# Kernel tuning notes

Hardware: AMD Instinct MI355X
Metric: run time of the kernel (lower is better)

## Reference

```python
import jax, jax.numpy as jnp
import numpy as np

ALPHA = 0.2        # LeakyReLU slope for attention scores (init arg alpha)
MLP_ALPHA = 0.01   # torch nn.LeakyReLU default slope in aftermlp
EPS = 1e-5         # nn.LayerNorm default eps


def leaky(x, a):
    return jnp.where(x >= 0, x, a * x)


def setup_inputs() -> dict:
    key = jax.random.key(0)
    ks = jax.random.split(key, 12)
    B, N, FIN, FOUT, K = 4, 4096, 256, 256, 64
    s = 0.05
    return {
        "h": jax.random.normal(ks[0], (B, N, FIN), jnp.float32),
        "adj": jax.random.uniform(ks[1], (B, N, N), jnp.float32),
        "W": jax.random.normal(ks[2], (FIN, FOUT), jnp.float32) * s,
        "a": jax.random.normal(ks[3], (FOUT, 1), jnp.float32) * s,
        "ln_g": jnp.ones((FOUT,), jnp.float32),
        "ln_b": jnp.zeros((FOUT,), jnp.float32),
        "W1": jax.random.normal(ks[4], (FOUT, FOUT), jnp.float32) * s,
        "b1": jnp.zeros((FOUT,), jnp.float32),
        "W2": jax.random.normal(ks[5], (FOUT, FOUT), jnp.float32) * s,
        "b2": jnp.zeros((FOUT,), jnp.float32),
        "W3": jax.random.normal(ks[6], (FOUT, FOUT), jnp.float32) * s,
        "b3": jnp.zeros((FOUT,), jnp.float32),
        "k": K,
    }


def reference(h, adj, W, a, ln_g, ln_b, W1, b1, W2, b2, W3, b3, k):
    # Wh: [B, N, F]
    Wh = h @ W
    B, N, Fd = Wh.shape
    C = N // k
    Whc = Wh.reshape(B, C, k, Fd)                       # [B, C, k, F]
    # a_input[b,c,i,j] = Wh[b,c,i]  =>  e[b,c,i,j] = leaky(Wh[b,c,i] . a)
    e = leaky(jnp.squeeze(Whc @ a, -1), ALPHA)          # [B, C, k]
    # block-diagonal chunks of adj: [B, C, k, k]
    idx = jnp.arange(C)
    blocks = adj.reshape(B, C, k, C, k)[:, idx, :, idx, :]  # [C, B, k, k]
    blocks = jnp.transpose(blocks, (1, 0, 2, 3))            # [B, C, k, k]
    scores = jax.nn.softmax(blocks * e[..., :, None], axis=-1)  # [B, C, k, k]
    out = jnp.einsum('bcij,bcjf->bcif', scores, Whc)    # [B, C, k, F]
    # aftermlp: Linear -> LeakyReLU(0.01) -> Linear -> LeakyReLU(0.01) -> Linear
    y = leaky(out @ W1 + b1, MLP_ALPHA)
    y = leaky(y @ W2 + b2, MLP_ALPHA)
    y = y @ W3 + b3
    # residual + LayerNorm over last dim
    z = y + out
    mu = jnp.mean(z, axis=-1, keepdims=True)
    var = jnp.var(z, axis=-1, keepdims=True)
    z = (z - mu) / jnp.sqrt(var + EPS) * ln_g + ln_b
    return z.reshape(B, N, Fd)
```

## Files before the change

kernel.cpp:

```cpp
#include <hip/hip_runtime.h>

typedef __bf16 bf16;
typedef __bf16 bf16x4 __attribute__((ext_vector_type(4)));
typedef __bf16 bf16x8 __attribute__((ext_vector_type(8)));
typedef float  f32x4  __attribute__((ext_vector_type(4)));

#define ALPHA 0.2f
#define MLP_ALPHA 0.01f
#define LN_EPS 1e-5f

constexpr int Bb = 4;
constexpr int Nn = 4096;
constexpr int Ff = 256;
constexpr int Kk = 64;
constexpr int Cc = 64;

__device__ __forceinline__ f32x4 MFMA(bf16x8 a, bf16x8 b, f32x4 c) {
  return __builtin_amdgcn_mfma_f32_16x16x32_bf16(a, b, c, 0, 0, 0);
}
__device__ __forceinline__ bf16x4 pack4(f32x4 v) {
  bf16x4 r; r[0]=(bf16)v[0]; r[1]=(bf16)v[1]; r[2]=(bf16)v[2]; r[3]=(bf16)v[3]; return r;
}
__device__ __forceinline__ int swz512(int i, int inrow) { return i*512 + (inrow ^ ((i & 15) << 4)); }
__device__ __forceinline__ int swz128(int f, int inrow) { return f*128 + (inrow ^ ((f & 7) << 4)); }

__global__ __launch_bounds__(256) void prep_weights(
    const float* __restrict__ W0, const float* __restrict__ W1,
    const float* __restrict__ W2, const float* __restrict__ W3,
    const float* __restrict__ a_vec,
    bf16* __restrict__ outw, float* __restrict__ wa)
{
  if (blockIdx.x == 128) {
    int k = threadIdx.x;
    const float* row = W0 + k * Ff;
    float s = 0.f;
    for (int j = 0; j < Ff; j += 4) {
      f32x4 wv = *(const f32x4*)(row + j);
      f32x4 av = *(const f32x4*)(a_vec + j);
      s += wv[0]*av[0] + wv[1]*av[1] + wv[2]*av[2] + wv[3]*av[3];
    }
    wa[k] = s;
    return;
  }
  int t = blockIdx.x * 256 + threadIdx.x;
  int l = t & 63, nt = (t >> 6) & 15, kt = (t >> 10) & 7, mat = t >> 13;
  const float* src = (mat==0) ? W0 : (mat==1) ? W1 : (mat==2) ? W2 : W3;
  int n  = nt*16 + (l & 15);
  int k0 = kt*32 + (l >> 4)*8;
  bf16x8 v;
  #pragma unroll
  for (int jj = 0; jj < 8; ++jj) v[jj] = (bf16)src[(k0 + jj)*Ff + n];
  *(bf16x8*)(outw + (size_t)t * 8) = v;
}

__device__ __forceinline__ void mlp_gemm(const bf16* __restrict__ wfrag, int mat,
                                         const bf16* inBuf, f32x4 acc[4][2],
                                         int w, int l)
{
  const int g = l >> 4, li = l & 15;
  #pragma unroll
  for (int kt = 0; kt < 8; ++kt) {
    bf16x8 af[2], bfr[4];
    #pragma unroll
    for (int r = 0; r < 2; ++r)
      af[r] = *(const bf16x8*)(wfrag + ((((size_t)mat*8 + kt)*16 + (w*2 + r))*64 + l)*8);
    #pragma unroll
    for (int nt = 0; nt < 4; ++nt) {
      int i = nt*16 + li;
      bfr[nt] = *(const bf16x8*)((const char*)inBuf + swz512(i, (kt*32 + g*8)*2));
    }
    #pragma unroll
    for (int nt = 0; nt < 4; ++nt)
      #pragma unroll
      for (int r = 0; r < 2; ++r)
        acc[nt][r] = MFMA(af[r], bfr[nt], acc[nt][r]);
  }
}

__device__ __forceinline__ void stage_store(f32x4 acc[4][2], const float* __restrict__ bias,
                                            bf16* outBuf, int w, int l)
{
  const int g = l >> 4, li = l & 15;
  float bv[2][4];
  #pragma unroll
  for (int r = 0; r < 2; ++r)
    #pragma unroll
    for (int e = 0; e < 4; ++e) bv[r][e] = bias[(w*2 + r)*16 + g*4 + e];
  #pragma unroll
  for (int nt = 0; nt < 4; ++nt) {
    int i = nt*16 + li;
    #pragma unroll
    for (int r = 0; r < 2; ++r) {
      f32x4 v;
      #pragma unroll
      for (int e = 0; e < 4; ++e) {
        float x = acc[nt][r][e] + bv[r][e];
        v[e] = (x >= 0.f) ? x : MLP_ALPHA * x;
      }
      int f0 = (w*2 + r)*16 + g*4;
      *(bf16x4*)((char*)outBuf + swz512(i, f0*2)) = pack4(v);
    }
  }
}

__global__ __launch_bounds__(512, 2) void gat_mfma(
    const float* __restrict__ h,   const float* __restrict__ adj,
    const float* __restrict__ gln, const float* __restrict__ bln,
    const float* __restrict__ b1,  const float* __restrict__ b2,
    const float* __restrict__ b3,
    const bf16* __restrict__ wfrag, const float* __restrict__ wa,
    float* __restrict__ out)
{
  __shared__ bf16 hbs[Kk * Ff];
  __shared__ bf16 bufA[Ff * Kk];
  __shared__ bf16 bufB[Kk * Ff];
  __shared__ bf16 sS[Kk * Kk];
  __shared__ float evec[Kk];
  __shared__ float lnS[Kk * 8], lnQ[Kk * 8];

  const int t = threadIdx.x, l = t & 63, w = t >> 6, g = l >> 4, li = l & 15;
  const int bc = blockIdx.x, b = bc >> 6, c = bc & 63;
  const size_t rbase = (size_t)b * Nn + c * Kk;

  float adjv[8];
  #pragma unroll
  for (int rr = 0; rr < 8; ++rr)
    adjv[rr] = adj[(rbase + w*8 + rr) * Nn + (size_t)c*Kk + l];

  {
    const int i  = t >> 3;
    const int k0 = (t & 7) * 32;
    const float* hp = h + (rbase + i) * Ff + k0;
    float p = 0.f;
    #pragma unroll
    for (int u = 0; u < 4; ++u) {
      f32x4 h0 = *(const f32x4*)(hp + u*8);
      f32x4 h1 = *(const f32x4*)(hp + u*8 + 4);
      f32x4 w0 = *(const f32x4*)(wa + k0 + u*8);
      f32x4 w1 = *(const f32x4*)(wa + k0 + u*8 + 4);
      p += h0[0]*w0[0] + h0[1]*w0[1] + h0[2]*w0[2] + h0[3]*w0[3]
         + h1[0]*w1[0] + h1[1]*w1[1] + h1[2]*w1[2] + h1[3]*w1[3];
      bf16x8 v;
      #pragma unroll
      for (int d = 0; d < 4; ++d) { v[d] = (bf16)h0[d]; v[4+d] = (bf16)h1[d]; }
      *(bf16x8*)((char*)hbs + swz512(i, (k0 + u*8)*2)) = v;
    }
    p += __shfl_xor(p, 1); p += __shfl_xor(p, 2); p += __shfl_xor(p, 4);
    if ((l & 7) == 0) evec[i] = (p >= 0.f) ? p : ALPHA * p;
  }
  __syncthreads();

  #pragma unroll
  for (int rr = 0; rr < 8; ++rr) {
    int i = w*8 + rr;
    float x = adjv[rr] * evec[i];
    float m = x;
    #pragma unroll
    for (int off = 32; off; off >>= 1) m = fmaxf(m, __shfl_xor(m, off));
    float pe = __expf(x - m);
    float s = pe;
    #pragma unroll
    for (int off = 32; off; off >>= 1) s += __shfl_xor(s, off);
    *(bf16*)((char*)sS + swz128(i, l*2)) = (bf16)(pe / s);
  }

  f32x4 acc1[2][4];
  #pragma unroll
  for (int q = 0; q < 2; ++q)
    #pragma unroll
    for (int rt = 0; rt < 4; ++rt) acc1[q][rt] = (f32x4){0.f,0.f,0.f,0.f};
  #pragma unroll
  for (int kt = 0; kt < 8; ++kt) {
    bf16x8 af[4];
    #pragma unroll
    for (int rt = 0; rt < 4; ++rt) {
      int i = rt*16 + li;
      af[rt] = *(const bf16x8*)((const char*)hbs + swz512(i, (kt*32 + g*8)*2));
    }
    #pragma unroll
    for (int q = 0; q < 2; ++q) {
      bf16x8 bfr = *(const bf16x8*)(wfrag + (((size_t)kt*16 + (w*2 + q))*64 + l)*8);
      #pragma unroll
      for (int rt = 0; rt < 4; ++rt) acc1[q][rt] = MFMA(af[rt], bfr, acc1[q][rt]);
    }
  }
  #pragma unroll
  for (int q = 0; q < 2; ++q) {
    int f = (w*2 + q)*16 + li;
    #pragma unroll
    for (int rt = 0; rt < 4; ++rt) {
      int j0 = rt*16 + g*4;
      *(bf16x4*)((char*)bufA + swz128(f, j0*2)) = pack4(acc1[q][rt]);
    }
  }
  __syncthreads();

  f32x4 xr[4][2];
  #pragma unroll
  for (int nt = 0; nt < 4; ++nt)
    #pragma unroll
    for (int r = 0; r < 2; ++r) xr[nt][r] = (f32x4){0.f,0.f,0.f,0.f};
  #pragma unroll
  for (int kt = 0; kt < 2; ++kt) {
    int koff = (kt*32 + g*8)*2;
    bf16x8 af[2], bfr[4];
    #pragma unroll
    for (int r = 0; r < 2; ++r) {
      int f = (w*2 + r)*16 + li;
      af[r] = *(const bf16x8*)((const char*)bufA + swz128(f, koff));
    }
    #pragma unroll
    for (int nt = 0; nt < 4; ++nt) {
      int i = nt*16 + li;
      bfr[nt] = *(const bf16x8*)((const char*)sS + swz128(i, koff));
    }
    #pragma unroll
    for (int nt = 0; nt < 4; ++nt)
      #pragma unroll
      for (int r = 0; r < 2; ++r) xr[nt][r] = MFMA(af[r], bfr[nt], xr[nt][r]);
  }
  #pragma unroll
  for (int nt = 0; nt < 4; ++nt) {
    int i = nt*16 + li;
    #pragma unroll
    for (int r = 0; r < 2; ++r) {
      int f0 = (w*2 + r)*16 + g*4;
      *(bf16x4*)((char*)bufB + swz512(i, f0*2)) = pack4(xr[nt][r]);
    }
  }
  __syncthreads();

  f32x4 acc3[4][2];
  #pragma unroll
  for (int nt = 0; nt < 4; ++nt)
    #pragma unroll
    for (int r = 0; r < 2; ++r) acc3[nt][r] = (f32x4){0.f,0.f,0.f,0.f};
  mlp_gemm(wfrag, 1, bufB, acc3, w, l);
  stage_store(acc3, b1, bufA, w, l);
  __syncthreads();

  #pragma unroll
  for (int nt = 0; nt < 4; ++nt)
    #pragma unroll
    for (int r = 0; r < 2; ++r) acc3[nt][r] = (f32x4){0.f,0.f,0.f,0.f};
  mlp_gemm(wfrag, 2, bufA, acc3, w, l);
  stage_store(acc3, b2, bufB, w, l);
  __syncthreads();

  #pragma unroll
  for (int nt = 0; nt < 4; ++nt)
    #pragma unroll
    for (int r = 0; r < 2; ++r) acc3[nt][r] = (f32x4){0.f,0.f,0.f,0.f};
  mlp_gemm(wfrag, 3, bufB, acc3, w, l);

  {
    float bv[2][4], gv[2][4], btv[2][4];
    #pragma unroll
    for (int r = 0; r < 2; ++r)
      #pragma unroll
      for (int e = 0; e < 4; ++e) {
        int f = (w*2 + r)*16 + g*4 + e;
        bv[r][e] = b3[f]; gv[r][e] = gln[f]; btv[r][e] = bln[f];
      }
    #pragma unroll
    for (int nt = 0; nt < 4; ++nt) {
      float s = 0.f, qq = 0.f;
      #pragma unroll
      for (int r = 0; r < 2; ++r)
        #pragma unroll
        for (int e = 0; e < 4; ++e) {
          float z = acc3[nt][r][e] + bv[r][e] + xr[nt][r][e];
          acc3[nt][r][e] = z;
          s += z; qq += z*z;
        }
      s  += __shfl_xor(s, 16);  s  += __shfl_xor(s, 32);
      qq += __shfl_xor(qq, 16); qq += __shfl_xor(qq, 32);
      if (g == 0) {
        int i = nt*16 + li;
        lnS[i*8 + w] = s;
        lnQ[i*8 + w] = qq;
      }
    }
    __syncthreads();
    #pragma unroll
    for (int nt = 0; nt < 4; ++nt) {
      int i = nt*16 + li;
      f32x4 s0 = *(const f32x4*)&lnS[i*8];
      f32x4 s1 = *(const f32x4*)&lnS[i*8 + 4];
      f32x4 q0 = *(const f32x4*)&lnQ[i*8];
      f32x4 q1 = *(const f32x4*)&lnQ[i*8 + 4];
      float s  = s0[0]+s0[1]+s0[2]+s0[3]+s1[0]+s1[1]+s1[2]+s1[3];
      float qq = q0[0]+q0[1]+q0[2]+q0[3]+q1[0]+q1[1]+q1[2]+q1[3];
      float mu  = s * (1.f/256.f);
      float var = qq * (1.f/256.f) - mu*mu;
      float rs  = rsqrtf(var + LN_EPS);
      #pragma unroll
      for (int r = 0; r < 2; ++r) {
        float4 o;
        o.x = (acc3[nt][r][0] - mu)*rs*gv[r][0] + btv[r][0];
        o.y = (acc3[nt][r][1] - mu)*rs*gv[r][1] + btv[r][1];
        o.z = (acc3[nt][r][2] - mu)*rs*gv[r][2] + btv[r][2];
        o.w = (acc3[nt][r][3] - mu)*rs*gv[r][3] + btv[r][3];
        *(float4*)&out[(rbase + i)*Ff + (w*2 + r)*16 + g*4] = o;
      }
    }
  }
}

extern "C" void kernel_launch(void* const* d_in, const int* in_sizes, int n_in,
                              void* d_out, int out_size, void* d_ws, size_t ws_size,
                              hipStream_t stream) {
  (void)in_sizes; (void)n_in; (void)out_size; (void)ws_size;
  bf16*  wfrag = (bf16*)d_ws;
  float* wa    = (float*)((char*)d_ws + 512*1024);
  prep_weights<<<dim3(129), dim3(256), 0, stream>>>(
      (const float*)d_in[2], (const float*)d_in[6],
      (const float*)d_in[8], (const float*)d_in[10],
      (const float*)d_in[3], wfrag, wa);
  gat_mfma<<<dim3(Bb * Cc), dim3(512), 0, stream>>>(
      (const float*)d_in[0],  (const float*)d_in[1],
      (const float*)d_in[4],  (const float*)d_in[5],
      (const float*)d_in[7],  (const float*)d_in[9],  (const float*)d_in[11],
      wfrag, wa, (float*)d_out);
}
```

Measured before the change: 36.82 us.

## Drop redundant barriers via shuffles and prefetch MLP weight fragments across syncs

The per-row attention scalar is now broadcast with a wavefront shuffle instead of going through shared memory, which removes one block-wide barrier. The barrier between writing bufA and the aggregation GEMM is also dropped, since each wave reads back only the rows it wrote. The first half of each MLP layer's weight fragments is loaded from global memory before the preceding barrier, so that load latency overlaps the sync wait. The cost is extra registers for the prefetched fragments, which could reduce occupancy at two blocks per CU.

```diff
diff --git a/kernel.cpp b/kernel.cpp
--- a/kernel.cpp
+++ b/kernel.cpp
@@ -53,53 +53,40 @@
   *(bf16x8*)(outw + (size_t)t * 8) = v;
 }
 
-__device__ __forceinline__ void mlp_gemm(const bf16* __restrict__ wfrag, int mat,
-                                         const bf16* inBuf, f32x4 acc[4][2],
-                                         int w, int l)
+__device__ __forceinline__ void prefetch_af(const bf16* __restrict__ wfrag, int mat,
+                                            bf16x8 pf[4][2], int w, int l) {
+  #pragma unroll
+  for (int kt = 0; kt < 4; ++kt)
+    #pragma unroll
+    for (int r = 0; r < 2; ++r)
+      pf[kt][r] = *(const bf16x8*)(wfrag + ((((size_t)mat*8 + kt)*16 + (w*2 + r))*64 + l)*8);
+}
+
+__device__ __forceinline__ void mlp_stage(const bf16* __restrict__ wfrag, int mat,
+                                          const bf16* inB, f32x4 acc[4][2],
+                                          bf16x8 pf[4][2], int w, int l)
 {
   const int g = l >> 4, li = l & 15;
   #pragma unroll
   for (int kt = 0; kt < 8; ++kt) {
-    bf16x8 af[2], bfr[4];
-    #pragma unroll
-    for (int r = 0; r < 2; ++r)
-      af[r] = *(const bf16x8*)(wfrag + ((((size_t)mat*8 + kt)*16 + (w*2 + r))*64 + l)*8);
+    bf16x8 af[2];
+    if (kt < 4) { af[0] = pf[kt][0]; af[1] = pf[kt][1]; }
+    else {
+      #pragma unroll
+      for (int r = 0; r < 2; ++r)
+        af[r] = *(const bf16x8*)(wfrag + ((((size_t)mat*8 + kt)*16 + (w*2 + r))*64 + l)*8);
+    }
+    bf16x8 bfr[4];
     #pragma unroll
     for (int nt = 0; nt < 4; ++nt) {
       int i = nt*16 + li;
-      bfr[nt] = *(const bf16x8*)((const char*)inBuf + swz512(i, (kt*32 + g*8)*2));
+      bfr[nt] = *(const bf16x8*)((const char*)inB + swz512(i, (kt*32 + g*8)*2));
     }
     #pragma unroll
     for (int nt = 0; nt < 4; ++nt)
       #pragma unroll
       for (int r = 0; r < 2; ++r)
         acc[nt][r] = MFMA(af[r], bfr[nt], acc[nt][r]);
-  }
-}
-
-__device__ __forceinline__ void stage_store(f32x4 acc[4][2], const float* __restrict__ bias,
-                                            bf16* outBuf, int w, int l)
-{
-  const int g = l >> 4, li = l & 15;
-  float bv[2][4];
-  #pragma unroll
-  for (int r = 0; r < 2; ++r)
-    #pragma unroll
-    for (int e = 0; e < 4; ++e) bv[r][e] = bias[(w*2 + r)*16 + g*4 + e];
-  #pragma unroll
-  for (int nt = 0; nt < 4; ++nt) {
-    int i = nt*16 + li;
-    #pragma unroll
-    for (int r = 0; r < 2; ++r) {
-      f32x4 v;
-      #pragma unroll
-      for (int e = 0; e < 4; ++e) {
-        float x = acc[nt][r][e] + bv[r][e];
-        v[e] = (x >= 0.f) ? x : MLP_ALPHA * x;
-      }
-      int f0 = (w*2 + r)*16 + g*4;
-      *(bf16x4*)((char*)outBuf + swz512(i, f0*2)) = pack4(v);
-    }
   }
 }
 
@@ -115,7 +102,6 @@
   __shared__ bf16 bufA[Ff * Kk];
   __shared__ bf16 bufB[Kk * Ff];
   __shared__ bf16 sS[Kk * Kk];
-  __shared__ float evec[Kk];
   __shared__ float lnS[Kk * 8], lnQ[Kk * 8];
 
   const int t = threadIdx.x, l = t & 63, w = t >> 6, g = l >> 4, li = l & 15;
@@ -127,6 +113,7 @@
   for (int rr = 0; rr < 8; ++rr)
     adjv[rr] = adj[(rbase + w*8 + rr) * Nn + (size_t)c*Kk + l];
 
+  float pl;
   {
     const int i  = t >> 3;
     const int k0 = (t & 7) * 32;
@@ -146,14 +133,14 @@
       *(bf16x8*)((char*)hbs + swz512(i, (k0 + u*8)*2)) = v;
     }
     p += __shfl_xor(p, 1); p += __shfl_xor(p, 2); p += __shfl_xor(p, 4);
-    if ((l & 7) == 0) evec[i] = (p >= 0.f) ? p : ALPHA * p;
-  }
-  __syncthreads();
+    pl = (p >= 0.f) ? p : ALPHA * p;
+  }
 
   #pragma unroll
   for (int rr = 0; rr < 8; ++rr) {
     int i = w*8 + rr;
-    float x = adjv[rr] * evec[i];
+    float e  = __shfl(pl, rr*8);
+    float x  = adjv[rr] * e;
     float m = x;
     #pragma unroll
     for (int off = 32; off; off >>= 1) m = fmaxf(m, __shfl_xor(m, off));
@@ -163,6 +150,7 @@
     for (int off = 32; off; off >>= 1) s += __shfl_xor(s, off);
     *(bf16*)((char*)sS + swz128(i, l*2)) = (bf16)(pe / s);
   }
+  __syncthreads();
 
   f32x4 acc1[2][4];
   #pragma unroll
@@ -193,7 +181,6 @@
       *(bf16x4*)((char*)bufA + swz128(f, j0*2)) = pack4(acc1[q][rt]);
     }
   }
-  __syncthreads();
 
   f32x4 xr[4][2];
   #pragma unroll
@@ -217,7 +204,8 @@
     #pragma unroll
     for (int nt = 0; nt < 4; ++nt)
       #pragma unroll
-      for (int r = 0; r < 2; ++r) xr[nt][r] = MFMA(af[r], bfr[nt], xr[nt][r]);
+      for (int r = 0; r < 2; ++r)
+        xr[nt][r] = MFMA(af[r], bfr[nt], xr[nt][r]);
   }
   #pragma unroll
   for (int nt = 0; nt < 4; ++nt) {
@@ -228,30 +216,63 @@
       *(bf16x4*)((char*)bufB + swz512(i, f0*2)) = pack4(xr[nt][r]);
     }
   }
+
+  bf16x8 pf[4][2];
+  f32x4 acc3[4][2];
+  prefetch_af(wfrag, 1, pf, w, l);
   __syncthreads();
 
-  f32x4 acc3[4][2];
   #pragma unroll
   for (int nt = 0; nt < 4; ++nt)
     #pragma unroll
     for (int r = 0; r < 2; ++r) acc3[nt][r] = (f32x4){0.f,0.f,0.f,0.f};
-  mlp_gemm(wfrag, 1, bufB, acc3, w, l);
-  stage_store(acc3, b1, bufA, w, l);
+  mlp_stage(wfrag, 1, bufB, acc3, pf, w, l);
+  #pragma unroll
+  for (int nt = 0; nt < 4; ++nt) {
+    int i = nt*16 + li;
+    #pragma unroll
+    for (int r = 0; r < 2; ++r) {
+      f32x4 v;
+      #pragma unroll
+      for (int e = 0; e < 4; ++e) {
+        float x = acc3[nt][r][e] + b1[(w*2 + r)*16 + g*4 + e];
+        v[e] = (x >= 0.f) ? x : MLP_ALPHA * x;
+      }
+      int f0 = (w*2 + r)*16 + g*4;
+      *(bf16x4*)((char*)bufA + swz512(i, f0*2)) = pack4(v);
+    }
+  }
+  prefetch_af(wfrag, 2, pf, w, l);
   __syncthreads();
 
   #pragma unroll
   for (int nt = 0; nt < 4; ++nt)
     #pragma unroll
     for (int r = 0; r < 2; ++r) acc3[nt][r] = (f32x4){0.f,0.f,0.f,0.f};
-  mlp_gemm(wfrag, 2, bufA, acc3, w, l);
-  stage_store(acc3, b2, bufB, w, l);
+  mlp_stage(wfrag, 2, bufA, acc3, pf, w, l);
+  #pragma unroll
+  for (int nt = 0; nt < 4; ++nt) {
+    int i = nt*16 + li;
+    #pragma unroll
+    for (int r = 0; r < 2; ++r) {
+      f32x4 v;
+      #pragma unroll
+      for (int e = 0; e < 4; ++e) {
+        float x = acc3[nt][r][e] + b2[(w*2 + r)*16 + g*4 + e];
+        v[e] = (x >= 0.f) ? x : MLP_ALPHA * x;
+      }
+      int f0 = (w*2 + r)*16 + g*4;
+      *(bf16x4*)((char*)bufB + swz512(i, f0*2)) = pack4(v);
+    }
+  }
+  prefetch_af(wfrag, 3, pf, w, l);
   __syncthreads();
 
   #pragma unroll
   for (int nt = 0; nt < 4; ++nt)
     #pragma unroll
     for (int r = 0; r < 2; ++r) acc3[nt][r] = (f32x4){0.f,0.f,0.f,0.f};
-  mlp_gemm(wfrag, 3, bufB, acc3, w, l);
+  mlp_stage(wfrag, 3, bufB, acc3, pf, w, l);
 
   {
     float bv[2][4], gv[2][4], btv[2][4];
```

New measurement: 37.26 us. About the same (+1.2%).
